# Optimization experiments

Measured on AMD Instinct MI355X. Metric: run time of the kernel, lower is better.

The kernel has to match this reference:

```python
import jax, jax.numpy as jnp
import numpy as np

K = 32        # num_classes
NQ = 16384    # num query samples
C = 512       # feature_dim
H_REF = 512   # refinement_net hidden
H_CONF = 256  # confidence_net hidden
NUM_STEPS = 3


def setup_inputs() -> dict:
    key = jax.random.key(0)
    ks = jax.random.split(key, 8)
    s = 0.02
    return {
        "prototypes": jax.random.normal(ks[0], (K, C), jnp.float32),
        "query_features": jax.random.normal(ks[1], (NQ, C), jnp.float32),
        "query_distances": jax.random.uniform(ks[2], (NQ, K), jnp.float32) * 10.0,
        "W1": jax.random.normal(ks[3], (2 * C, H_REF), jnp.float32) * s,
        "b1": jnp.zeros((H_REF,), jnp.float32),
        "W2": jax.random.normal(ks[4], (H_REF, C), jnp.float32) * s,
        "b2": jnp.zeros((C,), jnp.float32),
        "Wc1": jax.random.normal(ks[5], (2 * C, H_CONF), jnp.float32) * s,
        "bc1": jnp.zeros((H_CONF,), jnp.float32),
        "Wc2": jax.random.normal(ks[6], (H_CONF, 1), jnp.float32) * s,
        "bc2": jnp.zeros((1,), jnp.float32),
    }


def reference(prototypes, query_features, query_distances,
              W1, b1, W2, b2, Wc1, bc1, Wc2, bc2):
    # ---- refinement loop (3 steps, sequential in refined prototypes) ----
    refined = prototypes
    for step in range(NUM_STEPS):
        # soft assignments over classes; temperature = step + 1
        soft = jax.nn.softmax(-query_distances / (step + 1.0), axis=-1)  # (NQ, K)
        wsum = jnp.maximum(soft.sum(axis=0), 1e-6)                       # (K,)  clamp(min=1e-6)
        wmean = (soft.T @ query_features) / wsum[:, None]                # (K, C)
        concat = jnp.concatenate([refined, wmean], axis=-1)              # (K, 2C)
        h = jax.nn.relu(concat @ W1 + b1)                                # dropout is identity in eval
        refinement = h @ W2 + b2                                         # (K, C)
        refined = refined + 0.1 * refinement

    # ---- confidence scores: MLP on [proto, query] pairs, mean over queries ----
    # Split first-layer weight into proto half and query half to avoid
    # materializing the (K, NQ, 2C) concat explicitly (same math).
    Wp, Wq = Wc1[:C], Wc1[C:]
    hp = prototypes @ Wp          # (K, H_CONF)
    hq = query_features @ Wq      # (NQ, H_CONF)
    hidden = jax.nn.relu(hp[:, None, :] + hq[None, :, :] + bc1)  # (K, NQ, H_CONF)
    conf = jax.nn.sigmoid(hidden @ Wc2 + bc2)                    # (K, NQ, 1)
    confidence_scores = conf.reshape(K, -1).mean(axis=1)         # (K,)

    return refined, confidence_scores
```

## Files before the change

kernel.cpp:

```cpp
#include <hip/hip_runtime.h>

#define KP 32
#define NQg 16384
#define CD 512
#define HC 256
#define NS 3

typedef __attribute__((ext_vector_type(8))) short short8;
typedef __attribute__((ext_vector_type(4))) short short4_t;
typedef __attribute__((ext_vector_type(8))) __bf16 bf16x8;
typedef __attribute__((ext_vector_type(4))) float floatx4;

union S8B8 { short8 s; bf16x8 b; };

__device__ __forceinline__ short f2bf(float f) {
    union { float f; unsigned u; } v; v.f = f;
    unsigned r = v.u + 0x7fffu + ((v.u >> 16) & 1u);
    return (short)(r >> 16);
}
__device__ __forceinline__ float bf2f(short s) {
    union { unsigned u; float f; } v; v.u = ((unsigned)(unsigned short)s) << 16;
    return v.f;
}

__global__ __launch_bounds__(256) void k_A(const float* __restrict__ qd,
                                           const float* __restrict__ W1, const float* __restrict__ W2,
                                           const float* __restrict__ Wc1, const float* __restrict__ proto,
                                           const float* __restrict__ qf,
                                           short* __restrict__ softT,
                                           short* __restrict__ W1p, short* __restrict__ W2p,
                                           short* __restrict__ wqp, float* __restrict__ refined,
                                           short* __restrict__ qf2b, float* __restrict__ wmean,
                                           int* __restrict__ bar, float* __restrict__ dout) {
    int tid = threadIdx.x;
    int bid = blockIdx.x;
    if (bid < 64) {
        int q = bid * 256 + tid;
        float d[32];
        const float4* p = (const float4*)(qd + (size_t)q * 32);
#pragma unroll
        for (int j = 0; j < 8; j++) {
            float4 v = p[j];
            d[4 * j] = v.x; d[4 * j + 1] = v.y; d[4 * j + 2] = v.z; d[4 * j + 3] = v.w;
        }
#pragma unroll
        for (int s = 0; s < 3; s++) {
            float inv = -1.0f / (float)(s + 1);
            float e[32];
            float sum = 0.f;
#pragma unroll
            for (int k = 0; k < 32; k++) { e[k] = __expf(d[k] * inv); sum += e[k]; }
            float r = 1.0f / sum;
#pragma unroll
            for (int k = 0; k < 32; k++)
                softT[(size_t)(s * 32 + k) * NQg + q] = f2bf(e[k] * r);
        }
        return;
    }
    if (bid < 3712) {
        if (bid == 64) {
            if (tid < 32) dout[16384 + tid] = 0.f;
            else if (tid < 40) bar[tid - 32] = 0;
        }
        int idx = (bid - 64) * 256 + tid;
        if (idx < 524288) {
            int k = idx >> 9, n = idx & 511;
            W1p[((size_t)(k >> 3) * 512 + n) * 8 + (k & 7)] = f2bf(W1[idx]);
        } else if (idx < 786432) {
            int j = idx - 524288;
            int k = j >> 9, n = j & 511;
            W2p[((size_t)(k >> 3) * 512 + n) * 8 + (k & 7)] = f2bf(W2[j]);
        } else if (idx < 917504) {
            int j = idx - 786432;
            int k = j >> 8, n = j & 255;
            wqp[((size_t)(k >> 3) * 256 + n) * 8 + (k & 7)] = f2bf(Wc1[(size_t)(512 + k) * 256 + n]);
        } else {
            int j = idx - 917504;
            refined[j] = proto[j];
        }
        return;
    }
    if (bid < 3904) {
        int idx = (bid - 3712) * 256 + tid;
        wmean[idx] = 0.f;
        return;
    }
    {
        int j = (bid - 3904) * 256 + tid;
        float4 v = *(const float4*)&qf[(size_t)j * 4];
        short4_t o;
        o[0] = f2bf(v.x); o[1] = f2bf(v.y); o[2] = f2bf(v.z); o[3] = f2bf(v.w);
        *(short4_t*)&qf2b[(size_t)j * 4] = o;
    }
}

__global__ __launch_bounds__(256) void k_B(const short* __restrict__ qf2b,
                                           const short* __restrict__ softT,
                                           const short* __restrict__ wqp,
                                           float* __restrict__ wmean,
                                           short* __restrict__ hq_g) {
    __shared__ short B_lds[128 * 40];
    int tid = threadIdx.x;
    int lane = tid & 63, w = tid >> 6;
    int ml = lane & 15, q8 = lane >> 4;

    if (blockIdx.x < 256) {
        int kc = blockIdx.x >> 2, ns = blockIdx.x & 3;
        int c0 = ns * 128;
        int qbase0 = kc * 256;
        int c_l = 2 * lane;
        int q_l = 8 * w;

        floatx4 acc[6][2];
#pragma unroll
        for (int mt = 0; mt < 6; mt++)
#pragma unroll
            for (int nt = 0; nt < 2; nt++) acc[mt][nt] = (floatx4){0.f, 0.f, 0.f, 0.f};

        for (int step = 0; step < 8; step++) {
            int qb = qbase0 + step * 32;
            short8 sA, sB;
#pragma unroll
            for (int i = 0; i < 8; i++) {
                unsigned u = *(const unsigned*)&qf2b[(size_t)(qb + q_l + i) * 512 + c0 + c_l];
                sA[i] = (short)(u & 0xffffu);
                sB[i] = (short)(u >> 16);
            }
            __syncthreads();
            *(short8*)&B_lds[c_l * 40 + q_l] = sA;
            *(short8*)&B_lds[(c_l + 1) * 40 + q_l] = sB;
            S8B8 a[6];
#pragma unroll
            for (int mt = 0; mt < 6; mt++)
                a[mt].s = *(const short8*)&softT[(size_t)(mt * 16 + ml) * NQg + qb + q8 * 8];
            __syncthreads();
#pragma unroll
            for (int nt = 0; nt < 2; nt++) {
                S8B8 b; b.s = *(short8*)&B_lds[(w * 32 + nt * 16 + ml) * 40 + q8 * 8];
#pragma unroll
                for (int mt = 0; mt < 6; mt++)
                    acc[mt][nt] = __builtin_amdgcn_mfma_f32_16x16x32_bf16(a[mt].b, b.b, acc[mt][nt], 0, 0, 0);
            }
        }
#pragma unroll
        for (int mt = 0; mt < 6; mt++) {
#pragma unroll
            for (int nt = 0; nt < 2; nt++) {
                int c = c0 + w * 32 + nt * 16 + ml;
#pragma unroll
                for (int r = 0; r < 4; r++) {
                    int m = mt * 16 + q8 * 4 + r;
                    atomicAdd(&wmean[(size_t)m * 512 + c], acc[mt][nt][r]);
                }
            }
        }
    } else {
        int m0 = (blockIdx.x - 256) * 64;
        int n0 = w * 64;
        floatx4 acc[4][4];
#pragma unroll
        for (int mt = 0; mt < 4; mt++)
#pragma unroll
            for (int nt = 0; nt < 4; nt++) acc[mt][nt] = (floatx4){0.f, 0.f, 0.f, 0.f};

#pragma unroll 4
        for (int kc = 0; kc < 512; kc += 32) {
            S8B8 a[4], b[4];
#pragma unroll
            for (int mt = 0; mt < 4; mt++)
                a[mt].s = *(const short8*)&qf2b[(size_t)(m0 + mt * 16 + ml) * 512 + kc + q8 * 8];
#pragma unroll
            for (int nt = 0; nt < 4; nt++)
                b[nt].s = *(const short8*)&wqp[((size_t)((kc >> 3) + q8) * 256 + n0 + nt * 16 + ml) * 8];
#pragma unroll
            for (int mt = 0; mt < 4; mt++)
#pragma unroll
                for (int nt = 0; nt < 4; nt++)
                    acc[mt][nt] = __builtin_amdgcn_mfma_f32_16x16x32_bf16(a[mt].b, b[nt].b, acc[mt][nt], 0, 0, 0);
        }
#pragma unroll
        for (int mt = 0; mt < 4; mt++)
#pragma unroll
            for (int nt = 0; nt < 4; nt++) {
                int col = n0 + nt * 16 + ml;
#pragma unroll
                for (int r = 0; r < 4; r++) {
                    int row = m0 + mt * 16 + q8 * 4 + r;
                    hq_g[(size_t)row * 256 + col] = f2bf(acc[mt][nt][r]);
                }
            }
    }
}

__global__ __launch_bounds__(256) void k_C(const short* __restrict__ softT,
                                           float* __restrict__ wmean,
                                           const float* __restrict__ proto,
                                           const float* __restrict__ Wc1,
                                           const float* __restrict__ bc1,
                                           float* __restrict__ hpb) {
    int tid = threadIdx.x;
    if (blockIdx.x < 96) {
        __shared__ float red[256];
        int sk = blockIdx.x;
        const short* row = softT + (size_t)sk * NQg;
        float s = 0.f;
#pragma unroll
        for (int j = 0; j < 8; j++) {
            short8 v = *(const short8*)&row[j * 2048 + tid * 8];
#pragma unroll
            for (int i = 0; i < 8; i++) s += bf2f(v[i]);
        }
        red[tid] = s;
        __syncthreads();
        for (int off = 128; off > 0; off >>= 1) {
            if (tid < off) red[tid] += red[tid + off];
            __syncthreads();
        }
        float inv = 1.0f / fmaxf(red[0], 1e-6f);
        wmean[(size_t)sk * 512 + tid] *= inv;
        wmean[(size_t)sk * 512 + tid + 256] *= inv;
    } else {
        int r = blockIdx.x - 96;
        float a = bc1[tid];
        for (int i = 0; i < 512; i++) a += proto[r * 512 + i] * Wc1[(size_t)i * 256 + tid];
        hpb[r * 256 + tid] = a;
    }
}

__device__ __forceinline__ void gbar(int* bar, int phase, int nblk) {
    __syncthreads();
    if (threadIdx.x == 0) {
        __threadfence();
        __hip_atomic_fetch_add(&bar[phase], 1, __ATOMIC_ACQ_REL, __HIP_MEMORY_SCOPE_AGENT);
        while (__hip_atomic_load(&bar[phase], __ATOMIC_ACQUIRE, __HIP_MEMORY_SCOPE_AGENT) < nblk)
            __builtin_amdgcn_s_sleep(1);
    }
    __syncthreads();
}

__global__ __launch_bounds__(256) void k_D(const float* __restrict__ wmean,
                                           const short* __restrict__ W1p,
                                           const float* __restrict__ b1,
                                           const short* __restrict__ W2p,
                                           const float* __restrict__ b2,
                                           float* __restrict__ refined,
                                           short* __restrict__ hb,
                                           int* __restrict__ bar,
                                           const short* __restrict__ hq_g,
                                           const float* __restrict__ hpb,
                                           const float* __restrict__ Wc2,
                                           const float* __restrict__ bc2p,
                                           float* __restrict__ dout) {
    __shared__ float smem[10880];
    int tid = threadIdx.x, lane = tid & 63, w = tid >> 6;
    int ml = lane & 15, q8 = lane >> 4;

    if (blockIdx.x < 16) {
        float (*red)[32][36] = (float(*)[32][36])smem;
        int nb = blockIdx.x;
        int phase = 0;
        for (int s = 0; s < 3; s++) {
            {
                const float* srcA = (w < 2) ? refined : (wmean + (size_t)s * 32 * 512 - 512);
                int kw = w * 256;
                floatx4 acc[2][2];
#pragma unroll
                for (int mt = 0; mt < 2; mt++)
#pragma unroll
                    for (int nt = 0; nt < 2; nt++) acc[mt][nt] = (floatx4){0.f, 0.f, 0.f, 0.f};
                for (int st = 0; st < 8; st++) {
                    int k0 = kw + st * 32 + q8 * 8;
                    S8B8 a[2];
#pragma unroll
                    for (int mt = 0; mt < 2; mt++) {
                        const float* p = &srcA[(size_t)(mt * 16 + ml) * 512 + k0];
                        float4 f0 = *(const float4*)p;
                        float4 f1 = *(const float4*)(p + 4);
                        short8 t;
                        t[0] = f2bf(f0.x); t[1] = f2bf(f0.y); t[2] = f2bf(f0.z); t[3] = f2bf(f0.w);
                        t[4] = f2bf(f1.x); t[5] = f2bf(f1.y); t[6] = f2bf(f1.z); t[7] = f2bf(f1.w);
                        a[mt].s = t;
                    }
#pragma unroll
                    for (int nt = 0; nt < 2; nt++) {
                        int n = nb * 32 + nt * 16 + ml;
                        S8B8 b; b.s = *(const short8*)&W1p[((size_t)(k0 >> 3) * 512 + n) * 8];
#pragma unroll
                        for (int mt = 0; mt < 2; mt++)
                            acc[mt][nt] = __builtin_amdgcn_mfma_f32_16x16x32_bf16(a[mt].b, b.b, acc[mt][nt], 0, 0, 0);
                    }
                }
                __syncthreads();
#pragma unroll
                for (int mt = 0; mt < 2; mt++)
#pragma unroll
                    for (int nt = 0; nt < 2; nt++)
#pragma unroll
                        for (int r = 0; r < 4; r++)
                            red[w][mt * 16 + q8 * 4 + r][nt * 16 + ml] = acc[mt][nt][r];
                __syncthreads();
                int m = tid >> 3, n0 = (tid & 7) * 4;
                short4_t o;
#pragma unroll
                for (int i = 0; i < 4; i++) {
                    float v = b1[nb * 32 + n0 + i];
#pragma unroll
                    for (int w4 = 0; w4 < 4; w4++) v += red[w4][m][n0 + i];
                    o[i] = f2bf(fmaxf(v, 0.f));
                }
                *(short4_t*)&hb[(size_t)m * 512 + nb * 32 + n0] = o;
            }
            gbar(bar, phase++, 16);
            {
                int kw = w * 128;
                floatx4 acc[2][2];
#pragma unroll
                for (int mt = 0; mt < 2; mt++)
#pragma unroll
                    for (int nt = 0; nt < 2; nt++) acc[mt][nt] = (floatx4){0.f, 0.f, 0.f, 0.f};
                for (int st = 0; st < 4; st++) {
                    int k0 = kw + st * 32 + q8 * 8;
                    S8B8 a[2];
#pragma unroll
                    for (int mt = 0; mt < 2; mt++)
                        a[mt].s = *(const short8*)&hb[(size_t)(mt * 16 + ml) * 512 + k0];
#pragma unroll
                    for (int nt = 0; nt < 2; nt++) {
                        int n = nb * 32 + nt * 16 + ml;
                        S8B8 b; b.s = *(const short8*)&W2p[((size_t)(k0 >> 3) * 512 + n) * 8];
#pragma unroll
                        for (int mt = 0; mt < 2; mt++)
                            acc[mt][nt] = __builtin_amdgcn_mfma_f32_16x16x32_bf16(a[mt].b, b.b, acc[mt][nt], 0, 0, 0);
                    }
                }
                __syncthreads();
#pragma unroll
                for (int mt = 0; mt < 2; mt++)
#pragma unroll
                    for (int nt = 0; nt < 2; nt++)
#pragma unroll
                        for (int r = 0; r < 4; r++)
                            red[w][mt * 16 + q8 * 4 + r][nt * 16 + ml] = acc[mt][nt][r];
                __syncthreads();
                int m = tid >> 3, n0 = (tid & 7) * 4;
#pragma unroll
                for (int i = 0; i < 4; i++) {
                    int c = nb * 32 + n0 + i;
                    float v = b2[c];
#pragma unroll
                    for (int w4 = 0; w4 < 4; w4++) v += red[w4][m][n0 + i];
                    float val = refined[(size_t)m * 512 + c] + 0.1f * v;
                    refined[(size_t)m * 512 + c] = val;
                    if (s == 2) dout[(size_t)m * 512 + c] = val;
                }
            }
            if (s < 2) gbar(bar, phase++, 16);
        }
    } else {
        float* hp_lds = smem;
        short* hq_lds = (short*)(smem + 8320);
        float* wc2s   = smem + 8320 + 2240;
        float* confl  = smem + 8320 + 2240 + 256;
        int q0 = (blockIdx.x - 16) * 16;

        wc2s[tid] = Wc2[tid];
        if (tid < 32) confl[tid] = 0.f;
#pragma unroll
        for (int i = 0; i < 8; i++) {
            int idx = i * 1024 + tid * 4;
            int r = idx >> 8, c = idx & 255;
            *(float4*)&hp_lds[r * 260 + c] = *(const float4*)&hpb[idx];
        }
        {
            const short* hqs = hq_g + (size_t)q0 * 256;
            int r = tid >> 4, c = (tid & 15) * 16;
            *(short8*)&hq_lds[r * 280 + c] = *(const short8*)&hqs[r * 256 + c];
            *(short8*)&hq_lds[r * 280 + c + 8] = *(const short8*)&hqs[r * 256 + c + 8];
        }
        __syncthreads();

        int q = tid & 15, kg = tid >> 4;
        int k0 = kg, k1 = kg + 16;
        float s0 = 0.f, s1 = 0.f;
        for (int h = 0; h < 256; h += 4) {
            uint2 hv = *(uint2*)&hq_lds[q * 280 + h];
            float f0 = __uint_as_float((hv.x & 0xffffu) << 16);
            float f1 = __uint_as_float(hv.x & 0xffff0000u);
            float f2 = __uint_as_float((hv.y & 0xffffu) << 16);
            float f3 = __uint_as_float(hv.y & 0xffff0000u);
            float4 p0 = *(float4*)&hp_lds[k0 * 260 + h];
            float4 p1 = *(float4*)&hp_lds[k1 * 260 + h];
            float4 wv = *(float4*)&wc2s[h];
            s0 += fmaxf(p0.x + f0, 0.f) * wv.x;
            s0 += fmaxf(p0.y + f1, 0.f) * wv.y;
            s0 += fmaxf(p0.z + f2, 0.f) * wv.z;
            s0 += fmaxf(p0.w + f3, 0.f) * wv.w;
            s1 += fmaxf(p1.x + f0, 0.f) * wv.x;
            s1 += fmaxf(p1.y + f1, 0.f) * wv.y;
            s1 += fmaxf(p1.z + f2, 0.f) * wv.z;
            s1 += fmaxf(p1.w + f3, 0.f) * wv.w;
        }
        float bc2 = bc2p[0];
        float v0 = 1.f / (1.f + __expf(-(s0 + bc2)));
        float v1 = 1.f / (1.f + __expf(-(s1 + bc2)));
        atomicAdd(&confl[k0], v0);
        atomicAdd(&confl[k1], v1);
        __syncthreads();
        if (tid < 32) atomicAdd(&dout[16384 + tid], confl[tid] * (1.0f / 16384.0f));
    }
}

extern "C" void kernel_launch(void* const* d_in, const int* in_sizes, int n_in,
                              void* d_out, int out_size, void* d_ws, size_t ws_size,
                              hipStream_t stream) {
    const float* proto = (const float*)d_in[0];
    const float* qf    = (const float*)d_in[1];
    const float* qd    = (const float*)d_in[2];
    const float* W1    = (const float*)d_in[3];
    const float* b1    = (const float*)d_in[4];
    const float* W2    = (const float*)d_in[5];
    const float* b2    = (const float*)d_in[6];
    const float* Wc1   = (const float*)d_in[7];
    const float* bc1   = (const float*)d_in[8];
    const float* Wc2   = (const float*)d_in[9];
    const float* bc2   = (const float*)d_in[10];
    float* out = (float*)d_out;

    float* ws = (float*)d_ws;
    short* softT   = (short*)ws;
    short* qf2b    = (short*)(ws + 786432);
    float* wmean   = ws + 4980736;
    float* refined = ws + 5029888;
    short* hb      = (short*)(ws + 5046272);
    short* W1p     = (short*)(ws + 5054464);
    short* W2p     = (short*)(ws + 5316608);
    short* wqp     = (short*)(ws + 5447680);
    float* hpb     = ws + 5513216;
    int*   bar     = (int*)(ws + 5521408);
    short* hq      = (short*)(ws + 5521416);

    k_A<<<12096, 256, 0, stream>>>(qd, W1, W2, Wc1, proto, qf, softT, W1p, W2p, wqp,
                                   refined, qf2b, wmean, bar, out);
    k_B<<<512, 256, 0, stream>>>(qf2b, softT, wqp, wmean, hq);
    k_C<<<128, 256, 0, stream>>>(softT, wmean, proto, Wc1, bc1, hpb);
    k_D<<<1040, 256, 0, stream>>>(wmean, W1p, b1, W2p, b2, refined, hb, bar,
                                  hq, hpb, Wc2, bc2, out);
}
```

Measured before the change: 188.8 us.

## Register-tile confidence pair loop over 64 queries per block with warp reduction

The confidence branch of k_D now handles 64 queries per block instead of 16, so the grid shrinks from 1040 to 272 blocks. Each thread computes a 4-class by 2-query register tile, which reuses each LDS load across more FMAs. hp is converted to bf16 in LDS to save space. Per-block LDS atomics are replaced by a shuffle reduction with fewer global atomics. The costs are bf16 rounding of hp, which changes numerics slightly, and fewer blocks in flight, which lowers parallelism.

```diff
diff --git a/kernel.cpp b/kernel.cpp
--- a/kernel.cpp
+++ b/kernel.cpp
@@ -22,6 +22,8 @@
     union { unsigned u; float f; } v; v.u = ((unsigned)(unsigned short)s) << 16;
     return v.f;
 }
+__device__ __forceinline__ float bflo(unsigned u) { return __uint_as_float(u << 16); }
+__device__ __forceinline__ float bfhi(unsigned u) { return __uint_as_float(u & 0xffff0000u); }
 
 __global__ __launch_bounds__(256) void k_A(const float* __restrict__ qd,
                                            const float* __restrict__ W1, const float* __restrict__ W2,
@@ -251,7 +253,7 @@
                                            const float* __restrict__ Wc2,
                                            const float* __restrict__ bc2p,
                                            float* __restrict__ dout) {
-    __shared__ float smem[10880];
+    __shared__ float smem[12736];
     int tid = threadIdx.x, lane = tid & 63, w = tid >> 6;
     int ml = lane & 15, q8 = lane >> 4;
 
@@ -357,56 +359,79 @@
             if (s < 2) gbar(bar, phase++, 16);
         }
     } else {
-        float* hp_lds = smem;
-        short* hq_lds = (short*)(smem + 8320);
-        float* wc2s   = smem + 8320 + 2240;
-        float* confl  = smem + 8320 + 2240 + 256;
-        int q0 = (blockIdx.x - 16) * 16;
+        short* hq_s = (short*)smem;
+        short* hp_s = (short*)(smem + 8320);
+        float* wc2s = smem + 12480;
+        int q0 = (blockIdx.x - 16) * 64;
 
         wc2s[tid] = Wc2[tid];
-        if (tid < 32) confl[tid] = 0.f;
 #pragma unroll
         for (int i = 0; i < 8; i++) {
-            int idx = i * 1024 + tid * 4;
-            int r = idx >> 8, c = idx & 255;
-            *(float4*)&hp_lds[r * 260 + c] = *(const float4*)&hpb[idx];
-        }
-        {
-            const short* hqs = hq_g + (size_t)q0 * 256;
-            int r = tid >> 4, c = (tid & 15) * 16;
-            *(short8*)&hq_lds[r * 280 + c] = *(const short8*)&hqs[r * 256 + c];
-            *(short8*)&hq_lds[r * 280 + c + 8] = *(const short8*)&hqs[r * 256 + c + 8];
+            int idx = i * 256 + tid;
+            int r = idx >> 6, c = (idx & 63) * 4;
+            float4 v = *(const float4*)&hpb[r * 256 + c];
+            short4_t o;
+            o[0] = f2bf(v.x); o[1] = f2bf(v.y); o[2] = f2bf(v.z); o[3] = f2bf(v.w);
+            *(short4_t*)&hp_s[r * 260 + c] = o;
+        }
+#pragma unroll
+        for (int i = 0; i < 8; i++) {
+            int idx = i * 256 + tid;
+            int r = idx >> 5, c = (idx & 31) * 8;
+            short8 v = *(const short8*)&hq_g[(size_t)(q0 + r) * 256 + c];
+            short4_t lo = {v[0], v[1], v[2], v[3]};
+            short4_t hi = {v[4], v[5], v[6], v[7]};
+            *(short4_t*)&hq_s[r * 260 + c] = lo;
+            *(short4_t*)&hq_s[r * 260 + c + 4] = hi;
         }
         __syncthreads();
 
-        int q = tid & 15, kg = tid >> 4;
-        int k0 = kg, k1 = kg + 16;
-        float s0 = 0.f, s1 = 0.f;
+        int kg = tid >> 5, qg = tid & 31;
+        int k4 = kg * 4;
+        float acc[4][2];
+#pragma unroll
+        for (int i = 0; i < 4; i++) { acc[i][0] = 0.f; acc[i][1] = 0.f; }
+
         for (int h = 0; h < 256; h += 4) {
-            uint2 hv = *(uint2*)&hq_lds[q * 280 + h];
-            float f0 = __uint_as_float((hv.x & 0xffffu) << 16);
-            float f1 = __uint_as_float(hv.x & 0xffff0000u);
-            float f2 = __uint_as_float((hv.y & 0xffffu) << 16);
-            float f3 = __uint_as_float(hv.y & 0xffff0000u);
-            float4 p0 = *(float4*)&hp_lds[k0 * 260 + h];
-            float4 p1 = *(float4*)&hp_lds[k1 * 260 + h];
             float4 wv = *(float4*)&wc2s[h];
-            s0 += fmaxf(p0.x + f0, 0.f) * wv.x;
-            s0 += fmaxf(p0.y + f1, 0.f) * wv.y;
-            s0 += fmaxf(p0.z + f2, 0.f) * wv.z;
-            s0 += fmaxf(p0.w + f3, 0.f) * wv.w;
-            s1 += fmaxf(p1.x + f0, 0.f) * wv.x;
-            s1 += fmaxf(p1.y + f1, 0.f) * wv.y;
-            s1 += fmaxf(p1.z + f2, 0.f) * wv.z;
-            s1 += fmaxf(p1.w + f3, 0.f) * wv.w;
+            float hqv[2][4];
+#pragma unroll
+            for (int j = 0; j < 2; j++) {
+                uint2 u = *(uint2*)&hq_s[(qg + 32 * j) * 260 + h];
+                hqv[j][0] = bflo(u.x); hqv[j][1] = bfhi(u.x);
+                hqv[j][2] = bflo(u.y); hqv[j][3] = bfhi(u.y);
+            }
+#pragma unroll
+            for (int i = 0; i < 4; i++) {
+                uint2 u = *(uint2*)&hp_s[(k4 + i) * 260 + h];
+                float p0 = bflo(u.x), p1 = bfhi(u.x), p2 = bflo(u.y), p3 = bfhi(u.y);
+#pragma unroll
+                for (int j = 0; j < 2; j++) {
+                    acc[i][j] += fmaxf(p0 + hqv[j][0], 0.f) * wv.x;
+                    acc[i][j] += fmaxf(p1 + hqv[j][1], 0.f) * wv.y;
+                    acc[i][j] += fmaxf(p2 + hqv[j][2], 0.f) * wv.z;
+                    acc[i][j] += fmaxf(p3 + hqv[j][3], 0.f) * wv.w;
+                }
+            }
         }
         float bc2 = bc2p[0];
-        float v0 = 1.f / (1.f + __expf(-(s0 + bc2)));
-        float v1 = 1.f / (1.f + __expf(-(s1 + bc2)));
-        atomicAdd(&confl[k0], v0);
-        atomicAdd(&confl[k1], v1);
-        __syncthreads();
-        if (tid < 32) atomicAdd(&dout[16384 + tid], confl[tid] * (1.0f / 16384.0f));
+        float t[4];
+#pragma unroll
+        for (int i = 0; i < 4; i++) {
+            float v0 = 1.f / (1.f + __expf(-(acc[i][0] + bc2)));
+            float v1 = 1.f / (1.f + __expf(-(acc[i][1] + bc2)));
+            t[i] = v0 + v1;
+        }
+#pragma unroll
+        for (int m = 1; m <= 16; m <<= 1) {
+#pragma unroll
+            for (int i = 0; i < 4; i++) t[i] += __shfl_xor(t[i], m);
+        }
+        if ((tid & 31) == 0) {
+#pragma unroll
+            for (int i = 0; i < 4; i++)
+                atomicAdd(&dout[16384 + k4 + i], t[i] * (1.0f / 16384.0f));
+        }
     }
 }
 
@@ -443,6 +468,6 @@
                                    refined, qf2b, wmean, bar, out);
     k_B<<<512, 256, 0, stream>>>(qf2b, softT, wqp, wmean, hq);
     k_C<<<128, 256, 0, stream>>>(softT, wmean, proto, Wc1, bc1, hpb);
-    k_D<<<1040, 256, 0, stream>>>(wmean, W1p, b1, W2p, b2, refined, hb, bar,
-                                  hq, hpb, Wc2, bc2, out);
-}
+    k_D<<<272, 256, 0, stream>>>(wmean, W1p, b1, W2p, b2, refined, hb, bar,
+                                 hq, hpb, Wc2, bc2, out);
+}
```

Result: slower. 212.4 us (+12.5%).

## Fold normalization and hp projection into k_B, drop k_C launch

Applied to the files above, without the earlier changes.

The column-sum reduction and the hp = proto@Wc1 projection move out of k_C and into extra blocks of k_B, so one kernel launch goes away. The softmax-weight normalization now happens in k_D, which scales the wmean rows by a stored inverse sum when it converts them to bf16. This removes the separate read-modify-write pass over wmean. The confidence path also keeps hp in LDS as bf16 instead of fp32, which cuts shared memory per block and may raise occupancy, at some cost in precision on hp.

```diff
diff --git a/kernel.cpp b/kernel.cpp
--- a/kernel.cpp
+++ b/kernel.cpp
@@ -22,6 +22,8 @@
     union { unsigned u; float f; } v; v.u = ((unsigned)(unsigned short)s) << 16;
     return v.f;
 }
+__device__ __forceinline__ float bflo(unsigned u) { return __uint_as_float(u << 16); }
+__device__ __forceinline__ float bfhi(unsigned u) { return __uint_as_float(u & 0xffff0000u); }
 
 __global__ __launch_bounds__(256) void k_A(const float* __restrict__ qd,
                                            const float* __restrict__ W1, const float* __restrict__ W2,
@@ -98,7 +100,12 @@
                                            const short* __restrict__ softT,
                                            const short* __restrict__ wqp,
                                            float* __restrict__ wmean,
-                                           short* __restrict__ hq_g) {
+                                           short* __restrict__ hq_g,
+                                           float* __restrict__ wsuminv,
+                                           const float* __restrict__ proto,
+                                           const float* __restrict__ Wc1,
+                                           const float* __restrict__ bc1,
+                                           float* __restrict__ hpb) {
     __shared__ short B_lds[128 * 40];
     int tid = threadIdx.x;
     int lane = tid & 63, w = tid >> 6;
@@ -154,7 +161,7 @@
                 }
             }
         }
-    } else {
+    } else if (blockIdx.x < 512) {
         int m0 = (blockIdx.x - 256) * 64;
         int n0 = w * 64;
         floatx4 acc[4][4];
@@ -189,19 +196,9 @@
                     hq_g[(size_t)row * 256 + col] = f2bf(acc[mt][nt][r]);
                 }
             }
-    }
-}
-
-__global__ __launch_bounds__(256) void k_C(const short* __restrict__ softT,
-                                           float* __restrict__ wmean,
-                                           const float* __restrict__ proto,
-                                           const float* __restrict__ Wc1,
-                                           const float* __restrict__ bc1,
-                                           float* __restrict__ hpb) {
-    int tid = threadIdx.x;
-    if (blockIdx.x < 96) {
-        __shared__ float red[256];
-        int sk = blockIdx.x;
+    } else if (blockIdx.x < 608) {
+        float* red = (float*)B_lds;
+        int sk = blockIdx.x - 512;
         const short* row = softT + (size_t)sk * NQg;
         float s = 0.f;
 #pragma unroll
@@ -216,11 +213,9 @@
             if (tid < off) red[tid] += red[tid + off];
             __syncthreads();
         }
-        float inv = 1.0f / fmaxf(red[0], 1e-6f);
-        wmean[(size_t)sk * 512 + tid] *= inv;
-        wmean[(size_t)sk * 512 + tid + 256] *= inv;
+        if (tid == 0) wsuminv[sk] = 1.0f / fmaxf(red[0], 1e-6f);
     } else {
-        int r = blockIdx.x - 96;
+        int r = blockIdx.x - 608;
         float a = bc1[tid];
         for (int i = 0; i < 512; i++) a += proto[r * 512 + i] * Wc1[(size_t)i * 256 + tid];
         hpb[r * 256 + tid] = a;
@@ -239,6 +234,7 @@
 }
 
 __global__ __launch_bounds__(256) void k_D(const float* __restrict__ wmean,
+                                           const float* __restrict__ wsuminv,
                                            const short* __restrict__ W1p,
                                            const float* __restrict__ b1,
                                            const short* __restrict__ W2p,
@@ -251,7 +247,7 @@
                                            const float* __restrict__ Wc2,
                                            const float* __restrict__ bc2p,
                                            float* __restrict__ dout) {
-    __shared__ float smem[10880];
+    __shared__ float smem[6688];
     int tid = threadIdx.x, lane = tid & 63, w = tid >> 6;
     int ml = lane & 15, q8 = lane >> 4;
 
@@ -262,6 +258,11 @@
         for (int s = 0; s < 3; s++) {
             {
                 const float* srcA = (w < 2) ? refined : (wmean + (size_t)s * 32 * 512 - 512);
+                float iv0 = 1.f, iv1 = 1.f;
+                if (w >= 2) {
+                    iv0 = wsuminv[s * 32 + ml];
+                    iv1 = wsuminv[s * 32 + 16 + ml];
+                }
                 int kw = w * 256;
                 floatx4 acc[2][2];
 #pragma unroll
@@ -273,12 +274,15 @@
                     S8B8 a[2];
 #pragma unroll
                     for (int mt = 0; mt < 2; mt++) {
+                        float sc = mt ? iv1 : iv0;
                         const float* p = &srcA[(size_t)(mt * 16 + ml) * 512 + k0];
                         float4 f0 = *(const float4*)p;
                         float4 f1 = *(const float4*)(p + 4);
                         short8 t;
-                        t[0] = f2bf(f0.x); t[1] = f2bf(f0.y); t[2] = f2bf(f0.z); t[3] = f2bf(f0.w);
-                        t[4] = f2bf(f1.x); t[5] = f2bf(f1.y); t[6] = f2bf(f1.z); t[7] = f2bf(f1.w);
+                        t[0] = f2bf(f0.x * sc); t[1] = f2bf(f0.y * sc);
+                        t[2] = f2bf(f0.z * sc); t[3] = f2bf(f0.w * sc);
+                        t[4] = f2bf(f1.x * sc); t[5] = f2bf(f1.y * sc);
+                        t[6] = f2bf(f1.z * sc); t[7] = f2bf(f1.w * sc);
                         a[mt].s = t;
                     }
 #pragma unroll
@@ -357,19 +361,22 @@
             if (s < 2) gbar(bar, phase++, 16);
         }
     } else {
-        float* hp_lds = smem;
-        short* hq_lds = (short*)(smem + 8320);
-        float* wc2s   = smem + 8320 + 2240;
-        float* confl  = smem + 8320 + 2240 + 256;
+        short* hq_lds = (short*)smem;
+        short* hp_s   = (short*)smem + 4480;
+        float* wc2s   = smem + 6400;
+        float* confl  = smem + 6656;
         int q0 = (blockIdx.x - 16) * 16;
 
         wc2s[tid] = Wc2[tid];
         if (tid < 32) confl[tid] = 0.f;
 #pragma unroll
         for (int i = 0; i < 8; i++) {
-            int idx = i * 1024 + tid * 4;
-            int r = idx >> 8, c = idx & 255;
-            *(float4*)&hp_lds[r * 260 + c] = *(const float4*)&hpb[idx];
+            int idx = i * 256 + tid;
+            int r = idx >> 6, c = (idx & 63) * 4;
+            float4 v = *(const float4*)&hpb[r * 256 + c];
+            short4_t o;
+            o[0] = f2bf(v.x); o[1] = f2bf(v.y); o[2] = f2bf(v.z); o[3] = f2bf(v.w);
+            *(short4_t*)&hp_s[r * 260 + c] = o;
         }
         {
             const short* hqs = hq_g + (size_t)q0 * 256;
@@ -384,21 +391,18 @@
         float s0 = 0.f, s1 = 0.f;
         for (int h = 0; h < 256; h += 4) {
             uint2 hv = *(uint2*)&hq_lds[q * 280 + h];
-            float f0 = __uint_as_float((hv.x & 0xffffu) << 16);
-            float f1 = __uint_as_float(hv.x & 0xffff0000u);
-            float f2 = __uint_as_float((hv.y & 0xffffu) << 16);
-            float f3 = __uint_as_float(hv.y & 0xffff0000u);
-            float4 p0 = *(float4*)&hp_lds[k0 * 260 + h];
-            float4 p1 = *(float4*)&hp_lds[k1 * 260 + h];
+            float f0 = bflo(hv.x), f1 = bfhi(hv.x), f2 = bflo(hv.y), f3 = bfhi(hv.y);
+            uint2 u0 = *(uint2*)&hp_s[k0 * 260 + h];
+            uint2 u1 = *(uint2*)&hp_s[k1 * 260 + h];
             float4 wv = *(float4*)&wc2s[h];
-            s0 += fmaxf(p0.x + f0, 0.f) * wv.x;
-            s0 += fmaxf(p0.y + f1, 0.f) * wv.y;
-            s0 += fmaxf(p0.z + f2, 0.f) * wv.z;
-            s0 += fmaxf(p0.w + f3, 0.f) * wv.w;
-            s1 += fmaxf(p1.x + f0, 0.f) * wv.x;
-            s1 += fmaxf(p1.y + f1, 0.f) * wv.y;
-            s1 += fmaxf(p1.z + f2, 0.f) * wv.z;
-            s1 += fmaxf(p1.w + f3, 0.f) * wv.w;
+            s0 += fmaxf(bflo(u0.x) + f0, 0.f) * wv.x;
+            s0 += fmaxf(bfhi(u0.x) + f1, 0.f) * wv.y;
+            s0 += fmaxf(bflo(u0.y) + f2, 0.f) * wv.z;
+            s0 += fmaxf(bfhi(u0.y) + f3, 0.f) * wv.w;
+            s1 += fmaxf(bflo(u1.x) + f0, 0.f) * wv.x;
+            s1 += fmaxf(bfhi(u1.x) + f1, 0.f) * wv.y;
+            s1 += fmaxf(bflo(u1.y) + f2, 0.f) * wv.z;
+            s1 += fmaxf(bfhi(u1.y) + f3, 0.f) * wv.w;
         }
         float bc2 = bc2p[0];
         float v0 = 1.f / (1.f + __expf(-(s0 + bc2)));
@@ -437,12 +441,12 @@
     short* wqp     = (short*)(ws + 5447680);
     float* hpb     = ws + 5513216;
     int*   bar     = (int*)(ws + 5521408);
-    short* hq      = (short*)(ws + 5521416);
+    float* wsuminv = ws + 5521416;
+    short* hq      = (short*)(ws + 5521536);
 
     k_A<<<12096, 256, 0, stream>>>(qd, W1, W2, Wc1, proto, qf, softT, W1p, W2p, wqp,
                                    refined, qf2b, wmean, bar, out);
-    k_B<<<512, 256, 0, stream>>>(qf2b, softT, wqp, wmean, hq);
-    k_C<<<128, 256, 0, stream>>>(softT, wmean, proto, Wc1, bc1, hpb);
-    k_D<<<1040, 256, 0, stream>>>(wmean, W1p, b1, W2p, b2, refined, hb, bar,
+    k_B<<<640, 256, 0, stream>>>(qf2b, softT, wqp, wmean, hq, wsuminv, proto, Wc1, bc1, hpb);
+    k_D<<<1040, 256, 0, stream>>>(wmean, wsuminv, W1p, b1, W2p, b2, refined, hb, bar,
                                   hq, hpb, Wc2, bc2, out);
 }
```

Result: faster. 175.5 us (-7.1%).
